# Kernel optimization log

Hardware: AMD Instinct MI355X
Metric: run time of the kernel (lower is better)

The kernel has to match this reference:

```python
import jax, jax.numpy as jnp
import numpy as np

N, E, B = 100000, 640000, 256
F_IN, HID, HEADS = 128, 128, 4
C = HID // HEADS  # 32 channels per head
NEG_SLOPE = 0.2


def _p(key, shape, scale=0.1):
    return (jax.random.normal(key, shape) * scale).astype(jnp.float32)


def setup_inputs() -> dict:
    key = jax.random.key(0)
    ks = jax.random.split(key, 24)
    inp = {
        "x": jax.random.normal(ks[0], (N, F_IN), jnp.float32),
        "edge_index": jax.random.randint(ks[1], (2, E), 0, N),
        "batch": jnp.sort(jax.random.randint(ks[2], (N,), 0, B)),
        "w_in": _p(ks[3], (F_IN, HID)),
        "b_in": jnp.zeros((HID,), jnp.float32),
    }
    for i in range(3):
        inp[f"w{i}"] = _p(ks[4 + 4 * i], (HID, HEADS * C))
        inp[f"asrc{i}"] = _p(ks[5 + 4 * i], (HEADS, C))
        inp[f"adst{i}"] = _p(ks[6 + 4 * i], (HEADS, C))
        inp[f"b{i}"] = jnp.zeros((HID if i < 2 else C,), jnp.float32)
    inp["w_fp"] = _p(ks[20], (C, HID)); inp["b_fp"] = jnp.zeros((HID,), jnp.float32)
    inp["w_m1"] = _p(ks[21], (HID, HID // 2)); inp["b_m1"] = jnp.zeros((HID // 2,), jnp.float32)
    inp["w_m2"] = _p(ks[22], (HID // 2, 1)); inp["b_m2"] = jnp.zeros((1,), jnp.float32)
    return inp


def _gat(x, src, dst, W, a_src, a_dst, bias, concat):
    """PyG-style GATConv (edge_dim=None, eval mode, self-loops pre-appended)."""
    n = x.shape[0]
    H, Ch = a_src.shape
    h = (x @ W).reshape(n, H, Ch)                     # [N,H,C]
    al_s = (h * a_src).sum(-1)                        # [N,H]
    al_d = (h * a_dst).sum(-1)                        # [N,H]
    logit = jax.nn.leaky_relu(al_s[src] + al_d[dst], NEG_SLOPE)  # [Etot,H]
    # segment softmax over incoming edges of each dst node
    m = jax.ops.segment_max(logit, dst, num_segments=n)
    e = jnp.exp(logit - m[dst])
    s = jax.ops.segment_sum(e, dst, num_segments=n)
    alpha = e / (s[dst] + 1e-16)                      # [Etot,H]
    out = jax.ops.segment_sum(h[src] * alpha[:, :, None], dst, num_segments=n)  # [N,H,C]
    out = out.reshape(n, H * Ch) if concat else out.mean(axis=1)
    return out + bias


def reference(x, edge_index, batch, w_in, b_in,
              w0, asrc0, adst0, b0, w1, asrc1, adst1, b1, w2, asrc2, adst2, b2,
              w_fp, b_fp, w_m1, b_m1, w_m2, b_m2):
    n = x.shape[0]
    loops = jnp.arange(n, dtype=edge_index.dtype)
    src = jnp.concatenate([edge_index[0], loops])     # add self loops (PyG default)
    dst = jnp.concatenate([edge_index[1], loops])
    h = x @ w_in + b_in
    h = jax.nn.elu(_gat(h, src, dst, w0, asrc0, adst0, b0, True))
    h = jax.nn.elu(_gat(h, src, dst, w1, asrc1, adst1, b1, True))
    h = jax.nn.elu(_gat(h, src, dst, w2, asrc2, adst2, b2, False))  # [N,C]
    cnt = jax.ops.segment_sum(jnp.ones((n,), h.dtype), batch, num_segments=B)
    pooled = jax.ops.segment_sum(h, batch, num_segments=B) / jnp.maximum(cnt, 1.0)[:, None]
    out = pooled @ w_fp + b_fp                        # final_proj (out dim 32 != 128)
    hm = jax.nn.relu(out @ w_m1 + b_m1)
    return hm @ w_m2 + b_m2                           # [B,1]
```

## Files before the change

kernel.cpp:

```cpp
#include <hip/hip_runtime.h>

#define NEG 0.2f

typedef short s16x8 __attribute__((ext_vector_type(8)));
typedef float f32x4 __attribute__((ext_vector_type(4)));

__device__ __forceinline__ float lrelu(float x) { return x >= 0.f ? x : NEG * x; }
__device__ __forceinline__ float elu1(float x) { return x > 0.f ? x : __expf(x) - 1.f; }

__device__ __forceinline__ unsigned bf16rn(float f) {
    unsigned u = __float_as_uint(f);
    u += 0x7fffu + ((u >> 16) & 1u);
    return u >> 16;
}
__device__ __forceinline__ float bf16tof(ushort h) {
    return __uint_as_float(((unsigned)h) << 16);
}
__device__ __forceinline__ float bf16lo(unsigned u) { return __uint_as_float(u << 16); }
__device__ __forceinline__ float bf16hi(unsigned u) { return __uint_as_float(u & 0xffff0000u); }

__global__ void hist_kernel(const int* __restrict__ dst, int e, int n, int* __restrict__ deg) {
    int p = blockIdx.x & 7;
    int s = blockIdx.x >> 3;
    int nslices = gridDim.x >> 3;
    int rng = (n + 7) >> 3;
    int lo = p * rng, hi = min(n, lo + rng);
    int chunk = (e + nslices - 1) / nslices;
    int i0 = s * chunk, i1 = min(e, i0 + chunk);
    for (int i = i0 + threadIdx.x; i < i1; i += blockDim.x) {
        int d = dst[i];
        if (d >= lo && d < hi) atomicAdd(&deg[d], 1);
    }
}

__device__ __forceinline__ int waveIncScanI(int v, int lane) {
#pragma unroll
    for (int off = 1; off < 64; off <<= 1) {
        int u = __shfl_up(v, off);
        if (lane >= off) v += u;
    }
    return v;
}

__global__ void scan1_kernel(const int* __restrict__ deg, int nk,
                             int* __restrict__ rowp, int* __restrict__ bsums) {
    int t = threadIdx.x;
    int base = blockIdx.x * 2048 + t * 8;
    int vals[8];
    int sum = 0;
#pragma unroll
    for (int i = 0; i < 8; ++i) {
        int idx = base + i;
        int v = (idx < nk) ? deg[idx] : 0;
        vals[i] = sum;
        sum += v;
    }
    int lane = t & 63, w = t >> 6;
    int inc = waveIncScanI(sum, lane);
    __shared__ int wsums[4];
    if (lane == 63) wsums[w] = inc;
    __syncthreads();
    int wpre = 0;
#pragma unroll
    for (int i = 0; i < 3; ++i) wpre += (i < w) ? wsums[i] : 0;
    int exc = wpre + inc - sum;
#pragma unroll
    for (int i = 0; i < 8; ++i) {
        int idx = base + i;
        if (idx < nk) rowp[idx] = exc + vals[i];
    }
    if (t == 255) bsums[blockIdx.x] = wpre + inc;
}

__global__ void scan3_kernel(int* __restrict__ rowp, const int* __restrict__ bsums,
                             int nk, int total, int* __restrict__ cursor) {
    int g = blockIdx.x;
    __shared__ int spre;
    if (threadIdx.x < 64) {
        int lane = threadIdx.x;
        int v = 0;
        for (int base = lane; base < g; base += 64) v += bsums[base];
#pragma unroll
        for (int off = 32; off > 0; off >>= 1) v += __shfl_xor(v, off);
        if (lane == 0) spre = v;
    }
    __syncthreads();
    int pre = spre;
    int base = g * 2048 + threadIdx.x * 8;
#pragma unroll
    for (int i = 0; i < 8; ++i) {
        int idx = base + i;
        if (idx < nk) {
            int v = rowp[idx] + pre;
            rowp[idx] = v;
            cursor[idx] = v;
        } else if (idx == nk) {
            rowp[nk] = total;
        }
    }
}

__global__ void fill_kernel(const int* __restrict__ src, const int* __restrict__ dst, int e,
                            int n, int* __restrict__ cursor, int* __restrict__ col) {
    int p = blockIdx.x & 7;
    int s = blockIdx.x >> 3;
    int nslices = gridDim.x >> 3;
    int rng = (n + 7) >> 3;
    int lo = p * rng, hi = min(n, lo + rng);
    int chunk = (e + nslices - 1) / nslices;
    int i0 = s * chunk, i1 = min(e, i0 + chunk);
    for (int i = i0 + threadIdx.x; i < i1; i += blockDim.x) {
        int d = dst[i];
        if (d >= lo && d < hi) {
            int pos = atomicAdd(&cursor[d], 1);
            col[pos] = src[i];
        }
    }
}

__global__ void wpack_kernel(const float* __restrict__ w_in, const float* __restrict__ w0,
                             const float* __restrict__ w1, const float* __restrict__ w2,
                             const float* __restrict__ b_in,
                             ushort* __restrict__ whi, ushort* __restrict__ wlo,
                             float* __restrict__ beff) {
    int idx = blockIdx.x * 256 + threadIdx.x;
    if (idx >= 3 * 16384) return;
    int layer = idx >> 14, e = idx & 16383;
    int k = e >> 7, c = e & 127;
    float wv;
    if (layer == 0) {
        float s = 0.f;
        for (int m = 0; m < 128; ++m) s += w_in[k * 128 + m] * w0[m * 128 + c];
        wv = s;
    } else {
        const float* W = (layer == 1) ? w1 : w2;
        wv = W[e];
    }
    ushort hi = (ushort)bf16rn(wv);
    ushort lo = (ushort)bf16rn(wv - bf16tof(hi));
    int kt = k >> 5, kk = k & 31, j = kk & 7;
    int ln = ((kk >> 3) << 4) | (c & 15);
    int ntg = c >> 4;
    int pos = (layer << 14) + (((kt << 3) + ntg) * 64 + ln) * 8 + j;
    whi[pos] = hi;
    wlo[pos] = lo;
    if (idx < 128) {
        float s = 0.f;
        for (int m = 0; m < 128; ++m) s += b_in[m] * w0[m * 128 + idx];
        beff[idx] = s;
    }
}

template <bool BIAS, bool AL, bool ABF16>
__global__ __launch_bounds__(512, 4) void gemm_mfma_kernel(
    const void* __restrict__ Av, const ushort* __restrict__ whi, const ushort* __restrict__ wlo,
    const float* __restrict__ bias, ushort* __restrict__ outb, int n, int ntiles,
    const float* __restrict__ asrc, const float* __restrict__ adst,
    float* __restrict__ als, float* __restrict__ ald) {
    __shared__ s16x8 ahi[2][4][64];
    __shared__ s16x8 alo[2][4][64];
    int t = threadIdx.x;
    int wid = t >> 6, lane = t & 63;
    int ntp = wid & 3;
    int mhalf = wid >> 2;

    const s16x8* wph = (const s16x8*)whi;
    const s16x8* wpl = (const s16x8*)wlo;
    s16x8 wh[4][2], wl[4][2];
#pragma unroll
    for (int kt = 0; kt < 4; ++kt)
#pragma unroll
        for (int j = 0; j < 2; ++j) {
            int ntg = ntp * 2 + j;
            wh[kt][j] = wph[((kt << 3) + ntg) * 64 + lane];
            wl[kt][j] = wpl[((kt << 3) + ntg) * 64 + lane];
        }

    int c0 = ntp * 32 + (lane & 15);
    int c1 = c0 + 16;
    float bv0 = 0.f, bv1 = 0.f;
    if (BIAS) { bv0 = bias[c0]; bv1 = bias[c1]; }
    float as0 = 0.f, as1 = 0.f, ad0 = 0.f, ad1 = 0.f;
    if (AL) {
        as0 = asrc[ntp * 32 + (lane & 15)];
        as1 = asrc[ntp * 32 + 16 + (lane & 15)];
        ad0 = adst[ntp * 32 + (lane & 15)];
        ad1 = adst[ntp * 32 + 16 + (lane & 15)];
    }

    int srow = t >> 4, skoct = t & 15;
    int smh = srow >> 4, skt = skoct >> 2;
    int sln = ((skoct & 3) << 4) | (srow & 15);

    for (int tile = blockIdx.x; tile < ntiles; tile += gridDim.x) {
        int r0 = tile * 32;
        {
            int gr = r0 + srow;
            if (ABF16) {
                const ushort* Ab = (const ushort*)Av;
                s16x8 hi = {0, 0, 0, 0, 0, 0, 0, 0};
                if (gr < n) hi = *(const s16x8*)(Ab + (size_t)gr * 128 + skoct * 8);
                ahi[smh][skt][sln] = hi;
            } else {
                const float* Af = (const float*)Av;
                float4 v0 = make_float4(0.f, 0.f, 0.f, 0.f), v1 = v0;
                if (gr < n) {
                    const float4* rp = (const float4*)(Af + (size_t)gr * 128 + skoct * 8);
                    v0 = rp[0];
                    v1 = rp[1];
                }
                float f[8] = {v0.x, v0.y, v0.z, v0.w, v1.x, v1.y, v1.z, v1.w};
                s16x8 hi, lo;
#pragma unroll
                for (int j = 0; j < 8; ++j) {
                    ushort h = (ushort)bf16rn(f[j]);
                    hi[j] = (short)h;
                    lo[j] = (short)bf16rn(f[j] - bf16tof(h));
                }
                ahi[smh][skt][sln] = hi;
                alo[smh][skt][sln] = lo;
            }
        }
        __syncthreads();

        f32x4 acc0 = {0.f, 0.f, 0.f, 0.f};
        f32x4 acc1 = {0.f, 0.f, 0.f, 0.f};
#pragma unroll
        for (int kt = 0; kt < 4; ++kt) {
            s16x8 ah = ahi[mhalf][kt][lane];
            if (ABF16) {
                acc0 = __builtin_amdgcn_mfma_f32_16x16x32_bf16(ah, wh[kt][0], acc0, 0, 0, 0);
                acc0 = __builtin_amdgcn_mfma_f32_16x16x32_bf16(ah, wl[kt][0], acc0, 0, 0, 0);
                acc1 = __builtin_amdgcn_mfma_f32_16x16x32_bf16(ah, wh[kt][1], acc1, 0, 0, 0);
                acc1 = __builtin_amdgcn_mfma_f32_16x16x32_bf16(ah, wl[kt][1], acc1, 0, 0, 0);
            } else {
                s16x8 al = alo[mhalf][kt][lane];
                acc0 = __builtin_amdgcn_mfma_f32_16x16x32_bf16(ah, wh[kt][0], acc0, 0, 0, 0);
                acc0 = __builtin_amdgcn_mfma_f32_16x16x32_bf16(ah, wl[kt][0], acc0, 0, 0, 0);
                acc0 = __builtin_amdgcn_mfma_f32_16x16x32_bf16(al, wh[kt][0], acc0, 0, 0, 0);
                acc1 = __builtin_amdgcn_mfma_f32_16x16x32_bf16(ah, wh[kt][1], acc1, 0, 0, 0);
                acc1 = __builtin_amdgcn_mfma_f32_16x16x32_bf16(ah, wl[kt][1], acc1, 0, 0, 0);
                acc1 = __builtin_amdgcn_mfma_f32_16x16x32_bf16(al, wh[kt][1], acc1, 0, 0, 0);
            }
        }

        int rbase = r0 + mhalf * 16 + (lane >> 4) * 4;
#pragma unroll
        for (int i = 0; i < 4; ++i) {
            int r = rbase + i;
            float o0 = acc0[i] + bv0;
            float o1 = acc1[i] + bv1;
            if (r < n) {
                outb[(size_t)r * 128 + c0] = (ushort)bf16rn(o0);
                outb[(size_t)r * 128 + c1] = (ushort)bf16rn(o1);
            }
            if (AL) {
                float ps = o0 * as0 + o1 * as1;
                float pd = o0 * ad0 + o1 * ad1;
                ps += __shfl_xor(ps, 1); ps += __shfl_xor(ps, 2);
                ps += __shfl_xor(ps, 4); ps += __shfl_xor(ps, 8);
                pd += __shfl_xor(pd, 1); pd += __shfl_xor(pd, 2);
                pd += __shfl_xor(pd, 4); pd += __shfl_xor(pd, 8);
                if ((lane & 15) == 0 && r < n) {
                    als[r * 4 + ntp] = ps;
                    ald[r * 4 + ntp] = pd;
                }
            }
        }
        __syncthreads();
    }
}

template <bool CONCAT>
__global__ void agg_kernel(const ushort* __restrict__ hp, const float* __restrict__ als,
                           const float* __restrict__ ald_, const int* __restrict__ rowp,
                           const int* __restrict__ col, const float* __restrict__ bias,
                           ushort* __restrict__ outb, float* __restrict__ outf, int n) {
    int lane = threadIdx.x & 63;
    int hl = lane & 31;
    int wid = (blockIdx.x * blockDim.x + threadIdx.x) >> 6;
    int d = wid * 2 + (lane >> 5);
    bool valid = d < n;
    int dc = valid ? d : (n - 1);

    int h = hl >> 3;
    int c4 = hl * 4;
    int hh = hl & 3;
    int jl = hl >> 2;
    int bshf = lane & 32;

    int start = rowp[dc];
    int end = valid ? rowp[dc + 1] : start;

    float aldv_hh = ald_[dc * 4 + hh];
    float eself = __expf(lrelu(als[dc * 4 + h] + ald_[dc * 4 + h]));

    uint2 sv = *(const uint2*)(hp + (size_t)dc * 128 + c4);
    float a0 = eself * bf16lo(sv.x), a1 = eself * bf16hi(sv.x);
    float a2 = eself * bf16lo(sv.y), a3 = eself * bf16hi(sv.y);
    float esum = eself;

    int iters = (end - start + 7) >> 3;
    int oiters = __shfl_xor(iters, 32);
    int maxit = iters > oiters ? iters : oiters;
    unsigned nclamp = (unsigned)(n - 1);

    for (int it = 0; it < maxit; ++it) {
        int p0 = start + it * 8;
        bool act = p0 < end;
        int pc = act ? p0 : start;
        int4 ca = *(const int4*)(col + pc);
        int4 cb = *(const int4*)(col + pc + 4);
        int v0 = (jl & 4) ? cb.x : ca.x;
        int v1 = (jl & 4) ? cb.y : ca.y;
        int v2 = (jl & 4) ? cb.z : ca.z;
        int v3 = (jl & 4) ? cb.w : ca.w;
        int w0_ = (jl & 2) ? v2 : v0;
        int w1_ = (jl & 2) ? v3 : v1;
        unsigned se = (unsigned)((jl & 1) ? w1_ : w0_);
        se = se > nclamp ? nclamp : se;
        float ee = __expf(lrelu(als[(size_t)se * 4 + hh] + aldv_hh));
        ee = (act && (p0 + jl < end)) ? ee : 0.f;

#define EDGE(JJ, SRC)                                                              \
        {                                                                          \
            float ej = __shfl(ee, bshf | (JJ << 2) | h);                           \
            unsigned sju = (unsigned)(SRC);                                        \
            sju = sju > nclamp ? nclamp : sju;                                     \
            uint2 uv = *(const uint2*)(hp + (size_t)sju * 128 + c4);               \
            a0 += ej * bf16lo(uv.x); a1 += ej * bf16hi(uv.x);                      \
            a2 += ej * bf16lo(uv.y); a3 += ej * bf16hi(uv.y);                      \
            esum += ej;                                                            \
        }
        EDGE(0, ca.x) EDGE(1, ca.y) EDGE(2, ca.z) EDGE(3, ca.w)
        EDGE(4, cb.x) EDGE(5, cb.y) EDGE(6, cb.z) EDGE(7, cb.w)
#undef EDGE
    }

    float inv = 1.f / (esum + 1e-16f);
    a0 *= inv; a1 *= inv; a2 *= inv; a3 *= inv;
    if (CONCAT) {
        if (valid) {
            float o0 = elu1(a0 + bias[c4]);
            float o1 = elu1(a1 + bias[c4 + 1]);
            float o2 = elu1(a2 + bias[c4 + 2]);
            float o3 = elu1(a3 + bias[c4 + 3]);
            uint2 pk;
            pk.x = bf16rn(o0) | (bf16rn(o1) << 16);
            pk.y = bf16rn(o2) | (bf16rn(o3) << 16);
            *(uint2*)(outb + (size_t)d * 128 + c4) = pk;
        }
    } else {
        a0 += __shfl_xor(a0, 8); a0 += __shfl_xor(a0, 16);
        a1 += __shfl_xor(a1, 8); a1 += __shfl_xor(a1, 16);
        a2 += __shfl_xor(a2, 8); a2 += __shfl_xor(a2, 16);
        a3 += __shfl_xor(a3, 8); a3 += __shfl_xor(a3, 16);
        if (valid && hl < 8) {
            int cin = hl * 4;
            float4 o;
            o.x = elu1(a0 * 0.25f + bias[cin]);
            o.y = elu1(a1 * 0.25f + bias[cin + 1]);
            o.z = elu1(a2 * 0.25f + bias[cin + 2]);
            o.w = elu1(a3 * 0.25f + bias[cin + 3]);
            *(float4*)(outf + (size_t)d * 32 + cin) = o;
        }
    }
}

__global__ void poolmlp_kernel(const float* __restrict__ h2, const int* __restrict__ batch,
                               int n, const float* __restrict__ w_fp,
                               const float* __restrict__ b_fp, const float* __restrict__ w_m1,
                               const float* __restrict__ b_m1, const float* __restrict__ w_m2,
                               const float* __restrict__ b_m2, float* __restrict__ out) {
    int b = blockIdx.x, t = threadIdx.x;
    __shared__ int sb[2];
    if (t == 0) {
        int lo = 0, hi = n;
        while (lo < hi) { int mid = (lo + hi) >> 1; if (batch[mid] < b) lo = mid + 1; else hi = mid; }
        sb[0] = lo;
        int lo2 = lo, hi2 = n;
        while (lo2 < hi2) { int mid = (lo2 + hi2) >> 1; if (batch[mid] < b + 1) lo2 = mid + 1; else hi2 = mid; }
        sb[1] = lo2;
    }
    __syncthreads();
    int lo = sb[0], hi = sb[1];
    int c = t & 31, g = t >> 5;
    float acc = 0.f;
    for (int i = lo + g; i < hi; i += 8) acc += h2[(size_t)i * 32 + c];
    __shared__ float red[8][32];
    __shared__ float sp[32], so[128];
    red[g][c] = acc;
    __syncthreads();
    if (t < 32) {
        float s = 0.f;
#pragma unroll
        for (int g2 = 0; g2 < 8; ++g2) s += red[g2][t];
        float cnt = (float)(hi - lo);
        sp[t] = s / fmaxf(cnt, 1.f);
    }
    __syncthreads();
    if (t < 128) {
        float o = b_fp[t];
#pragma unroll 8
        for (int k = 0; k < 32; ++k) o += sp[k] * w_fp[k * 128 + t];
        so[t] = o;
    }
    __syncthreads();
    if (t < 64) {
        float hm = b_m1[t];
        for (int cc = 0; cc < 128; ++cc) hm += so[cc] * w_m1[cc * 64 + t];
        float v = fmaxf(hm, 0.f) * w_m2[t];
#pragma unroll
        for (int offd = 32; offd > 0; offd >>= 1) v += __shfl_down(v, offd);
        if (t == 0) out[b] = v + b_m2[0];
    }
}

extern "C" void kernel_launch(void* const* d_in, const int* in_sizes, int n_in,
                              void* d_out, int out_size, void* d_ws, size_t ws_size,
                              hipStream_t stream) {
    const float* x = (const float*)d_in[0];
    const int* ei = (const int*)d_in[1];
    const int* batch = (const int*)d_in[2];
    const float* w_in = (const float*)d_in[3];
    const float* b_in = (const float*)d_in[4];
    const float* w[3] = {(const float*)d_in[5], (const float*)d_in[9], (const float*)d_in[13]};
    const float* asrc[3] = {(const float*)d_in[6], (const float*)d_in[10], (const float*)d_in[14]};
    const float* adst[3] = {(const float*)d_in[7], (const float*)d_in[11], (const float*)d_in[15]};
    const float* bb[3] = {(const float*)d_in[8], (const float*)d_in[12], (const float*)d_in[16]};
    const float* w_fp = (const float*)d_in[17];
    const float* b_fp = (const float*)d_in[18];
    const float* w_m1 = (const float*)d_in[19];
    const float* b_m1 = (const float*)d_in[20];
    const float* w_m2 = (const float*)d_in[21];
    const float* b_m2 = (const float*)d_in[22];

    int n = in_sizes[0] / 128;
    int e = in_sizes[1] / 2;
    int B = out_size;

    char* wsb = (char*)d_ws;
    size_t off = 0;
    auto alloc = [&](size_t bytes) -> void* {
        void* p = wsb + off;
        off += (bytes + 255) & ~(size_t)255;
        return p;
    };
    ushort* hAu = (ushort*)alloc((size_t)n * 128 * 2);
    ushort* hBu = (ushort*)alloc((size_t)n * 128 * 2);
    float* h3 = (float*)alloc((size_t)n * 32 * 4);
    float* als = (float*)alloc((size_t)n * 4 * 4);
    float* ald = (float*)alloc((size_t)n * 4 * 4);
    int* deg = (int*)alloc((size_t)n * 4);
    int* rowp = (int*)alloc((size_t)(n + 1) * 4);
    int* col = (int*)alloc((size_t)(e + 8) * 4);
    int* bsums = (int*)alloc(4096);
    ushort* whi = (ushort*)alloc((size_t)3 * 16384 * 2);
    ushort* wlo = (ushort*)alloc((size_t)3 * 16384 * 2);
    float* beff = (float*)alloc(128 * 4);

    const int* srcp = ei;
    const int* dstp = ei + e;

    hipMemsetAsync(deg, 0, (size_t)n * 4, stream);
    hist_kernel<<<1024, 256, 0, stream>>>(dstp, e, n, deg);
    int nb = (n + 2047) / 2048;
    scan1_kernel<<<nb, 256, 0, stream>>>(deg, n, rowp, bsums);
    scan3_kernel<<<nb, 256, 0, stream>>>(rowp, bsums, n, e, deg);
    fill_kernel<<<1024, 256, 0, stream>>>(srcp, dstp, e, n, deg, col);

    wpack_kernel<<<192, 256, 0, stream>>>(w_in, w[0], w[1], w[2], b_in, whi, wlo, beff);

    int ntiles = (n + 31) / 32;
    int gblk = ntiles < 512 ? ntiles : 512;
    int gridAgg = (n + 7) / 8;

    gemm_mfma_kernel<true, true, false><<<gblk, 512, 0, stream>>>(
        x, whi, wlo, beff, hBu, n, ntiles, asrc[0], adst[0], als, ald);
    agg_kernel<true><<<gridAgg, 256, 0, stream>>>(hBu, als, ald, rowp, col, bb[0],
                                                  hAu, nullptr, n);

    for (int L = 1; L < 3; ++L) {
        gemm_mfma_kernel<false, true, true><<<gblk, 512, 0, stream>>>(
            hAu, whi + (size_t)L * 16384, wlo + (size_t)L * 16384, nullptr, hBu, n,
            ntiles, asrc[L], adst[L], als, ald);
        if (L < 2)
            agg_kernel<true><<<gridAgg, 256, 0, stream>>>(hBu, als, ald, rowp, col, bb[L],
                                                          hAu, nullptr, n);
        else
            agg_kernel<false><<<gridAgg, 256, 0, stream>>>(hBu, als, ald, rowp, col, bb[L],
                                                           nullptr, h3, n);
    }

    poolmlp_kernel<<<B, 256, 0, stream>>>(h3, batch, n, w_fp, b_fp, w_m1, b_m1, w_m2, b_m2,
                                          (float*)d_out);
}
```

Baseline: 287.8 us.

## Double-buffer GEMM input tiles and fold degree zeroing into weight-pack kernel

The MFMA GEMM now stages the next row tile into a second LDS buffer while computing on the current one, with one barrier per iteration instead of two. Launch bounds drop from 4 to 2 blocks per CU, which leaves more registers per thread but may reduce occupancy. The hipMemsetAsync of the degree array is removed: zeroing is done inside wpack_kernel, which now launches before the histogram, saving one launch. Issuing the next tile's global load before the current MFMAs could hide load latency, at the cost of doubled shared memory.

```diff
diff --git a/kernel.cpp b/kernel.cpp
--- a/kernel.cpp
+++ b/kernel.cpp
@@ -122,8 +122,10 @@
                              const float* __restrict__ w1, const float* __restrict__ w2,
                              const float* __restrict__ b_in,
                              ushort* __restrict__ whi, ushort* __restrict__ wlo,
-                             float* __restrict__ beff) {
+                             float* __restrict__ beff, int n, int* __restrict__ degz) {
     int idx = blockIdx.x * 256 + threadIdx.x;
+    int stride = gridDim.x * 256;
+    for (int i = idx; i < n; i += stride) degz[i] = 0;
     if (idx >= 3 * 16384) return;
     int layer = idx >> 14, e = idx & 16383;
     int k = e >> 7, c = e & 127;
@@ -152,13 +154,13 @@
 }
 
 template <bool BIAS, bool AL, bool ABF16>
-__global__ __launch_bounds__(512, 4) void gemm_mfma_kernel(
+__global__ __launch_bounds__(512, 2) void gemm_mfma_kernel(
     const void* __restrict__ Av, const ushort* __restrict__ whi, const ushort* __restrict__ wlo,
     const float* __restrict__ bias, ushort* __restrict__ outb, int n, int ntiles,
     const float* __restrict__ asrc, const float* __restrict__ adst,
     float* __restrict__ als, float* __restrict__ ald) {
-    __shared__ s16x8 ahi[2][4][64];
-    __shared__ s16x8 alo[2][4][64];
+    __shared__ s16x8 ahi[2][2][4][64];
+    __shared__ s16x8 alo[2][2][4][64];
     int t = threadIdx.x;
     int wid = t >> 6, lane = t & 63;
     int ntp = wid & 3;
@@ -192,49 +194,55 @@
     int smh = srow >> 4, skt = skoct >> 2;
     int sln = ((skoct & 3) << 4) | (srow & 15);
 
-    for (int tile = blockIdx.x; tile < ntiles; tile += gridDim.x) {
-        int r0 = tile * 32;
-        {
-            int gr = r0 + srow;
-            if (ABF16) {
-                const ushort* Ab = (const ushort*)Av;
-                s16x8 hi = {0, 0, 0, 0, 0, 0, 0, 0};
-                if (gr < n) hi = *(const s16x8*)(Ab + (size_t)gr * 128 + skoct * 8);
-                ahi[smh][skt][sln] = hi;
-            } else {
-                const float* Af = (const float*)Av;
-                float4 v0 = make_float4(0.f, 0.f, 0.f, 0.f), v1 = v0;
-                if (gr < n) {
-                    const float4* rp = (const float4*)(Af + (size_t)gr * 128 + skoct * 8);
-                    v0 = rp[0];
-                    v1 = rp[1];
-                }
-                float f[8] = {v0.x, v0.y, v0.z, v0.w, v1.x, v1.y, v1.z, v1.w};
-                s16x8 hi, lo;
-#pragma unroll
-                for (int j = 0; j < 8; ++j) {
-                    ushort h = (ushort)bf16rn(f[j]);
-                    hi[j] = (short)h;
-                    lo[j] = (short)bf16rn(f[j] - bf16tof(h));
-                }
-                ahi[smh][skt][sln] = hi;
-                alo[smh][skt][sln] = lo;
+    auto stage = [&](int tile, int bi) {
+        int gr = tile * 32 + srow;
+        if (ABF16) {
+            const ushort* Ab = (const ushort*)Av;
+            s16x8 hi = {0, 0, 0, 0, 0, 0, 0, 0};
+            if (gr < n) hi = *(const s16x8*)(Ab + (size_t)gr * 128 + skoct * 8);
+            ahi[bi][smh][skt][sln] = hi;
+        } else {
+            const float* Af = (const float*)Av;
+            float4 v0 = make_float4(0.f, 0.f, 0.f, 0.f), v1 = v0;
+            if (gr < n) {
+                const float4* rp = (const float4*)(Af + (size_t)gr * 128 + skoct * 8);
+                v0 = rp[0];
+                v1 = rp[1];
             }
-        }
-        __syncthreads();
+            float f[8] = {v0.x, v0.y, v0.z, v0.w, v1.x, v1.y, v1.z, v1.w};
+            s16x8 hi, lo;
+#pragma unroll
+            for (int j = 0; j < 8; ++j) {
+                ushort h = (ushort)bf16rn(f[j]);
+                hi[j] = (short)h;
+                lo[j] = (short)bf16rn(f[j] - bf16tof(h));
+            }
+            ahi[bi][smh][skt][sln] = hi;
+            alo[bi][smh][skt][sln] = lo;
+        }
+    };
+
+    int tile = blockIdx.x;
+    if (tile < ntiles) stage(tile, 0);
+    int cur = 0;
+    __syncthreads();
+
+    for (; tile < ntiles; tile += gridDim.x) {
+        int nxt = tile + gridDim.x;
+        if (nxt < ntiles) stage(nxt, cur ^ 1);
 
         f32x4 acc0 = {0.f, 0.f, 0.f, 0.f};
         f32x4 acc1 = {0.f, 0.f, 0.f, 0.f};
 #pragma unroll
         for (int kt = 0; kt < 4; ++kt) {
-            s16x8 ah = ahi[mhalf][kt][lane];
+            s16x8 ah = ahi[cur][mhalf][kt][lane];
             if (ABF16) {
                 acc0 = __builtin_amdgcn_mfma_f32_16x16x32_bf16(ah, wh[kt][0], acc0, 0, 0, 0);
                 acc0 = __builtin_amdgcn_mfma_f32_16x16x32_bf16(ah, wl[kt][0], acc0, 0, 0, 0);
                 acc1 = __builtin_amdgcn_mfma_f32_16x16x32_bf16(ah, wh[kt][1], acc1, 0, 0, 0);
                 acc1 = __builtin_amdgcn_mfma_f32_16x16x32_bf16(ah, wl[kt][1], acc1, 0, 0, 0);
             } else {
-                s16x8 al = alo[mhalf][kt][lane];
+                s16x8 al = alo[cur][mhalf][kt][lane];
                 acc0 = __builtin_amdgcn_mfma_f32_16x16x32_bf16(ah, wh[kt][0], acc0, 0, 0, 0);
                 acc0 = __builtin_amdgcn_mfma_f32_16x16x32_bf16(ah, wl[kt][0], acc0, 0, 0, 0);
                 acc0 = __builtin_amdgcn_mfma_f32_16x16x32_bf16(al, wh[kt][0], acc0, 0, 0, 0);
@@ -244,7 +252,7 @@
             }
         }
 
-        int rbase = r0 + mhalf * 16 + (lane >> 4) * 4;
+        int rbase = tile * 32 + mhalf * 16 + (lane >> 4) * 4;
 #pragma unroll
         for (int i = 0; i < 4; ++i) {
             int r = rbase + i;
@@ -268,6 +276,7 @@
             }
         }
         __syncthreads();
+        cur ^= 1;
     }
 }
 
@@ -462,14 +471,14 @@
     const int* srcp = ei;
     const int* dstp = ei + e;
 
-    hipMemsetAsync(deg, 0, (size_t)n * 4, stream);
+    wpack_kernel<<<192, 256, 0, stream>>>(w_in, w[0], w[1], w[2], b_in, whi, wlo, beff,
+                                          n, deg);
+
     hist_kernel<<<1024, 256, 0, stream>>>(dstp, e, n, deg);
     int nb = (n + 2047) / 2048;
     scan1_kernel<<<nb, 256, 0, stream>>>(deg, n, rowp, bsums);
     scan3_kernel<<<nb, 256, 0, stream>>>(rowp, bsums, n, e, deg);
     fill_kernel<<<1024, 256, 0, stream>>>(srcp, dstp, e, n, deg, col);
-
-    wpack_kernel<<<192, 256, 0, stream>>>(w_in, w[0], w[1], w[2], b_in, whi, wlo, beff);
 
     int ntiles = (n + 31) / 32;
     int gblk = ntiles < 512 ? ntiles : 512;
```

Result: no change. 282.7 us (median of 2 runs) (-1.8%).
